# Kernel optimization log

Measured on AMD Instinct MI355X. Metric: run time of the kernel, lower is better.

## Reference

```python
import jax, jax.numpy as jnp
import numpy as np

N, E, B = 100000, 1000000, 64
DIN, DS, H, NG = 128, 1024, 256, 20


def setup_inputs() -> dict:
    key = jax.random.key(0)
    ks = jax.random.split(key, 48)
    lin = lambda k, i, o: (jax.random.normal(k, (i, o), jnp.float32) / np.sqrt(i)).astype(jnp.float32)
    inp = {
        'x': jax.random.normal(ks[0], (N, DIN), jnp.float32),
        'edge_index': jax.random.randint(ks[1], (2, E), 0, N, jnp.int32),
        'batch': jnp.sort(jax.random.randint(ks[2], (N,), 0, B, jnp.int32)),
        'static_features': jax.random.normal(ks[3], (B, DS), jnp.float32),
        'temporal_feats': jax.random.normal(ks[4], (B, 5), jnp.float32),
        'type_idx': jax.random.randint(ks[5], (B,), 0, 10, jnp.int32),
        'type_emb': jax.random.normal(ks[6], (10, H), jnp.float32),
        # static encoder
        'Ws1': lin(ks[7], DS, H), 'bs1': jnp.zeros(H), 'Ws2': lin(ks[8], H, H), 'bs2': jnp.zeros(H),
        # 3 GCN convs
        'Wc1': lin(ks[9], DIN, H), 'bc1': jnp.zeros(H),
        'Wc2': lin(ks[10], H, H), 'bc2': jnp.zeros(H),
        'Wc3': lin(ks[11], H, H), 'bc3': jnp.zeros(H),
        # residual dim_match linears
        'Wd1': lin(ks[12], DIN, H), 'bd1': jnp.zeros(H),
        'Wd2': lin(ks[13], H, H), 'bd2': jnp.zeros(H),
        'Wd3': lin(ks[14], H, H), 'bd3': jnp.zeros(H),
        # temporal MLP (5 -> H//2 -> H)
        'Wt1': lin(ks[15], 5, H // 2), 'bt1': jnp.zeros(H // 2),
        'Wt2': lin(ks[16], H // 2, H), 'bt2': jnp.zeros(H),
        # pattern detector
        'Wp1': lin(ks[17], H, H // 2), 'bp1': jnp.zeros(H // 2),
        'Wp2': lin(ks[18], H // 2, H), 'bp2': jnp.zeros(H),
        # fusion (5H -> 2H -> H)
        'Wf1': lin(ks[19], 5 * H, 2 * H), 'bf1': jnp.zeros(2 * H),
        'Wf2': lin(ks[20], 2 * H, H), 'bf2': jnp.zeros(H),
        # heads
        'Wg': lin(ks[21], H, NG), 'bg': jnp.zeros(NG),
        'Wtp': lin(ks[22], H, 1), 'btp': jnp.zeros(1),
    }
    return inp


def reference(x, edge_index, batch, static_features, temporal_feats, type_idx, type_emb,
              Ws1, bs1, Ws2, bs2,
              Wc1, bc1, Wc2, bc2, Wc3, bc3,
              Wd1, bd1, Wd2, bd2, Wd3, bd3,
              Wt1, bt1, Wt2, bt2,
              Wp1, bp1, Wp2, bp2,
              Wf1, bf1, Wf2, bf2,
              Wg, bg, Wtp, btp):
    n = x.shape[0]
    b = static_features.shape[0]
    src, dst = edge_index[0], edge_index[1]
    # GCN symmetric norm with self-loops: deg = 1 + in-degree
    deg = 1.0 + jax.ops.segment_sum(jnp.ones(src.shape[0], x.dtype), dst, num_segments=n)
    dinv = deg ** -0.5
    ew = dinv[src] * dinv[dst]  # [E] edge norm weights

    def gcn(h_in, W, bias):
        h = h_in @ W  # [n, H]
        agg = jax.ops.segment_sum(h[src] * ew[:, None], dst, num_segments=n)
        return agg + h / deg[:, None] + bias  # neighbor agg + self-loop + bias

    # 3 GCN layers with residual dim_match (dropout is identity at inference)
    x1 = jax.nn.relu(gcn(x, Wc1, bc1)) + (x @ Wd1 + bd1)
    x2 = jax.nn.relu(gcn(x1, Wc2, bc2)) + (x1 @ Wd2 + bd2)
    x3 = jax.nn.relu(gcn(x2, Wc3, bc3)) + (x2 @ Wd3 + bd3)

    pat = jax.nn.relu(jax.nn.relu(x3 @ Wp1 + bp1) @ Wp2 + bp2)

    counts = jnp.maximum(jax.ops.segment_sum(jnp.ones(n, x.dtype), batch, num_segments=b), 1.0)
    graph_embed = jax.ops.segment_sum(x3, batch, num_segments=b) / counts[:, None]
    pattern_embed = jax.ops.segment_sum(pat, batch, num_segments=b) / counts[:, None]

    static_embed = jax.nn.relu(static_features @ Ws1 + bs1) @ Ws2 + bs2
    temporal_embed = jax.nn.relu(temporal_feats @ Wt1 + bt1) @ Wt2 + bt2
    type_embed = type_emb[type_idx]

    combined = jnp.concatenate([graph_embed, static_embed, temporal_embed, type_embed, pattern_embed], axis=1)
    fused = jax.nn.relu(combined @ Wf1 + bf1) @ Wf2 + bf2
    group_logits = fused @ Wg + bg
    time_pred = fused @ Wtp + btp
    return fused, group_logits, time_pred
```

## Files before the change

kernel.cpp:

```cpp
#include <hip/hip_runtime.h>

#define H 256

typedef __attribute__((ext_vector_type(8))) short bf16x8;
typedef __attribute__((ext_vector_type(4))) float f32x4;

__device__ __forceinline__ float b2f(ushort h) {
    return __uint_as_float(((unsigned)h) << 16);
}
__device__ __forceinline__ float b2f_lo(unsigned u) {
    return __uint_as_float(u << 16);
}
__device__ __forceinline__ float b2f_hi(unsigned u) {
    return __uint_as_float(u & 0xffff0000u);
}
__device__ __forceinline__ ushort f2bf(float f) {
    unsigned u = __float_as_uint(f);
    unsigned r = (u + 0x7FFF + ((u >> 16) & 1)) >> 16;
    return (ushort)r;
}
__device__ __forceinline__ unsigned pack2bf(float lo, float hi) {
    return (unsigned)f2bf(lo) | ((unsigned)f2bf(hi) << 16);
}

__device__ __forceinline__ void gload16(const ushort* g, const short* l) {
    __builtin_amdgcn_global_load_lds(
        (const __attribute__((address_space(1))) void*)(const void*)g,
        (__attribute__((address_space(3))) void*)(void*)l, 16, 0, 0);
}

__global__ __launch_bounds__(256) void k_zero2_i(int* p, int* q, int n) {
    int i = blockIdx.x * 256 + threadIdx.x;
    if (i < n) { p[i] = 0; q[i] = 0; }
}

__global__ __launch_bounds__(256) void k_zero_f(float* p, int n) {
    int i = blockIdx.x * 256 + threadIdx.x;
    if (i < n) p[i] = 0.f;
}

__global__ __launch_bounds__(256) void k_count_deg_i(const int* __restrict__ dst, int* cnt, int E) {
    int i = blockIdx.x * 256 + threadIdx.x;
    if (i < E) atomicAdd(&cnt[dst[i]], 1);
}

__global__ __launch_bounds__(256) void k_scan1(const int* __restrict__ cnt, int* __restrict__ partial,
                                               int* __restrict__ bsums, int N) {
    __shared__ int s[256];
    int t = threadIdx.x;
    int idx = blockIdx.x * 256 + t;
    int v = idx < N ? cnt[idx] : 0;
    s[t] = v;
    __syncthreads();
    for (int off = 1; off < 256; off <<= 1) {
        int add = (t >= off) ? s[t - off] : 0;
        __syncthreads();
        s[t] += add;
        __syncthreads();
    }
    if (idx < N) partial[idx] = s[t];
    if (t == 255) bsums[blockIdx.x] = s[t];
}

__global__ __launch_bounds__(1024) void k_scan2(int* bsums, int nb) {
    __shared__ int s[1024];
    int t = threadIdx.x;
    s[t] = (t < nb) ? bsums[t] : 0;
    __syncthreads();
    for (int off = 1; off < 1024; off <<= 1) {
        int add = (t >= off) ? s[t - off] : 0;
        __syncthreads();
        s[t] += add;
        __syncthreads();
    }
    if (t < nb) bsums[t] = s[t];
}

__global__ __launch_bounds__(256) void k_scan3(const int* __restrict__ partial, const int* __restrict__ bsums,
                                               const int* __restrict__ cnt,
                                               int* __restrict__ rowptr, float* __restrict__ dinv,
                                               float* __restrict__ selfw, int N) {
    int idx = blockIdx.x * 256 + threadIdx.x;
    if (idx < N) {
        int off = blockIdx.x > 0 ? bsums[blockIdx.x - 1] : 0;
        rowptr[idx + 1] = partial[idx] + off;
        if (idx == 0) rowptr[0] = 0;
        float d = 1.0f + (float)cnt[idx];
        dinv[idx] = rsqrtf(d);
        selfw[idx] = 1.0f / d;
    }
}

__global__ __launch_bounds__(256) void k_scatter(const int* __restrict__ src, const int* __restrict__ dst,
                                                 const float* __restrict__ dinv, const int* __restrict__ rowptr,
                                                 int* __restrict__ fill, int* __restrict__ esrc,
                                                 float* __restrict__ ewt, int E) {
    int e = blockIdx.x * 256 + threadIdx.x;
    if (e >= E) return;
    int s = src[e], d = dst[e];
    int pos = rowptr[d] + atomicAdd(&fill[d], 1);
    esrc[pos] = s;
    ewt[pos] = dinv[s] * dinv[d];
}

__device__ __forceinline__ void tcvt_one(long i, const float* __restrict__ W, ushort* __restrict__ Wt,
                                         int K, int M) {
    int k = (int)(i / M), m = (int)(i - (long)k * M);
    Wt[(size_t)m * K + k] = f2bf(W[(size_t)k * M + m]);
}

__global__ __launch_bounds__(256) void k_prep(
    const float* __restrict__ x, ushort* __restrict__ xh, long nx, int DIN,
    const float* __restrict__ Wc1, ushort* Wc1t, const float* __restrict__ Wd1, ushort* Wd1t,
    const float* __restrict__ Wc2, ushort* Wc2t, const float* __restrict__ Wd2, ushort* Wd2t,
    const float* __restrict__ Wc3, ushort* Wc3t, const float* __restrict__ Wd3, ushort* Wd3t,
    const float* __restrict__ Wp1, ushort* Wp1t, const float* __restrict__ Wp2, ushort* Wp2t) {
    long i = (long)blockIdx.x * 256 + threadIdx.x;
    if (i < nx) { xh[i] = f2bf(x[i]); return; }
    i -= nx;
    long n1 = (long)DIN * 256;
    if (i < n1) { tcvt_one(i, Wc1, Wc1t, DIN, 256); return; }
    i -= n1;
    if (i < n1) { tcvt_one(i, Wd1, Wd1t, DIN, 256); return; }
    i -= n1;
    if (i < 65536) { tcvt_one(i, Wc2, Wc2t, 256, 256); return; }
    i -= 65536;
    if (i < 65536) { tcvt_one(i, Wd2, Wd2t, 256, 256); return; }
    i -= 65536;
    if (i < 65536) { tcvt_one(i, Wc3, Wc3t, 256, 256); return; }
    i -= 65536;
    if (i < 65536) { tcvt_one(i, Wd3, Wd3t, 256, 256); return; }
    i -= 65536;
    if (i < 32768) { tcvt_one(i, Wp1, Wp1t, 256, 128); return; }
    i -= 32768;
    if (i < 32768) { tcvt_one(i, Wp2, Wp2t, 128, 256); return; }
}

__global__ __launch_bounds__(256) void k_gather_b4(const ushort* __restrict__ xin, const int* __restrict__ rowptr,
                                                   const int* __restrict__ esrc, const float* __restrict__ ewt,
                                                   const float* __restrict__ selfw, ushort* __restrict__ p,
                                                   int N, int SX, int SP) {
    int node = blockIdx.x * 4 + (threadIdx.x >> 6);
    if (node >= N) return;
    int c = (threadIdx.x & 63) << 2;
    ushort4 h = *(const ushort4*)(xin + (size_t)node * SX + c);
    float sw = selfw[node];
    float a0 = b2f(h.x) * sw, a1 = b2f(h.y) * sw, a2 = b2f(h.z) * sw, a3 = b2f(h.w) * sw;
    int j = rowptr[node], r1 = rowptr[node + 1];
    for (; j + 3 < r1; j += 4) {
        int s0 = esrc[j], s1 = esrc[j + 1], s2 = esrc[j + 2], s3 = esrc[j + 3];
        float w0 = ewt[j], w1 = ewt[j + 1], w2 = ewt[j + 2], w3 = ewt[j + 3];
        ushort4 v0 = *(const ushort4*)(xin + (size_t)s0 * SX + c);
        ushort4 v1 = *(const ushort4*)(xin + (size_t)s1 * SX + c);
        ushort4 v2 = *(const ushort4*)(xin + (size_t)s2 * SX + c);
        ushort4 v3 = *(const ushort4*)(xin + (size_t)s3 * SX + c);
        a0 += b2f(v0.x) * w0 + b2f(v1.x) * w1 + b2f(v2.x) * w2 + b2f(v3.x) * w3;
        a1 += b2f(v0.y) * w0 + b2f(v1.y) * w1 + b2f(v2.y) * w2 + b2f(v3.y) * w3;
        a2 += b2f(v0.z) * w0 + b2f(v1.z) * w1 + b2f(v2.z) * w2 + b2f(v3.z) * w3;
        a3 += b2f(v0.w) * w0 + b2f(v1.w) * w1 + b2f(v2.w) * w2 + b2f(v3.w) * w3;
    }
    for (; j < r1; ++j) {
        int s0 = esrc[j];
        float w0 = ewt[j];
        ushort4 v0 = *(const ushort4*)(xin + (size_t)s0 * SX + c);
        a0 += b2f(v0.x) * w0; a1 += b2f(v0.y) * w0; a2 += b2f(v0.z) * w0; a3 += b2f(v0.w) * w0;
    }
    ushort4 o;
    o.x = f2bf(a0); o.y = f2bf(a1); o.z = f2bf(a2); o.w = f2bf(a3);
    *(ushort4*)(p + (size_t)node * SP + c) = o;
}

__global__ __launch_bounds__(256) void k_gather_b2(const ushort* __restrict__ xin, const int* __restrict__ rowptr,
                                                   const int* __restrict__ esrc, const float* __restrict__ ewt,
                                                   const float* __restrict__ selfw, ushort* __restrict__ p,
                                                   int N, int SX, int SP) {
    int node = blockIdx.x * 16 + (threadIdx.x >> 4);
    bool act = node < N;
    int nn = act ? node : N - 1;
    int c = (threadIdx.x & 15) << 3;
    uint4 hv = *(const uint4*)(xin + (size_t)nn * SX + c);
    float sw = selfw[nn];
    float a0 = b2f_lo(hv.x) * sw, a1 = b2f_hi(hv.x) * sw;
    float a2 = b2f_lo(hv.y) * sw, a3 = b2f_hi(hv.y) * sw;
    float a4 = b2f_lo(hv.z) * sw, a5 = b2f_hi(hv.z) * sw;
    float a6 = b2f_lo(hv.w) * sw, a7 = b2f_hi(hv.w) * sw;
    int j = act ? rowptr[nn] : 0, r1 = act ? rowptr[nn + 1] : 0;
    for (; j + 3 < r1; j += 4) {
        int s0 = esrc[j], s1 = esrc[j + 1], s2 = esrc[j + 2], s3 = esrc[j + 3];
        float w0 = ewt[j], w1 = ewt[j + 1], w2 = ewt[j + 2], w3 = ewt[j + 3];
        uint4 v0 = *(const uint4*)(xin + (size_t)s0 * SX + c);
        uint4 v1 = *(const uint4*)(xin + (size_t)s1 * SX + c);
        uint4 v2 = *(const uint4*)(xin + (size_t)s2 * SX + c);
        uint4 v3 = *(const uint4*)(xin + (size_t)s3 * SX + c);
        a0 += b2f_lo(v0.x) * w0 + b2f_lo(v1.x) * w1 + b2f_lo(v2.x) * w2 + b2f_lo(v3.x) * w3;
        a1 += b2f_hi(v0.x) * w0 + b2f_hi(v1.x) * w1 + b2f_hi(v2.x) * w2 + b2f_hi(v3.x) * w3;
        a2 += b2f_lo(v0.y) * w0 + b2f_lo(v1.y) * w1 + b2f_lo(v2.y) * w2 + b2f_lo(v3.y) * w3;
        a3 += b2f_hi(v0.y) * w0 + b2f_hi(v1.y) * w1 + b2f_hi(v2.y) * w2 + b2f_hi(v3.y) * w3;
        a4 += b2f_lo(v0.z) * w0 + b2f_lo(v1.z) * w1 + b2f_lo(v2.z) * w2 + b2f_lo(v3.z) * w3;
        a5 += b2f_hi(v0.z) * w0 + b2f_hi(v1.z) * w1 + b2f_hi(v2.z) * w2 + b2f_hi(v3.z) * w3;
        a6 += b2f_lo(v0.w) * w0 + b2f_lo(v1.w) * w1 + b2f_lo(v2.w) * w2 + b2f_lo(v3.w) * w3;
        a7 += b2f_hi(v0.w) * w0 + b2f_hi(v1.w) * w1 + b2f_hi(v2.w) * w2 + b2f_hi(v3.w) * w3;
    }
    for (; j < r1; ++j) {
        int s0 = esrc[j];
        float w0 = ewt[j];
        uint4 v0 = *(const uint4*)(xin + (size_t)s0 * SX + c);
        a0 += b2f_lo(v0.x) * w0; a1 += b2f_hi(v0.x) * w0;
        a2 += b2f_lo(v0.y) * w0; a3 += b2f_hi(v0.y) * w0;
        a4 += b2f_lo(v0.z) * w0; a5 += b2f_hi(v0.z) * w0;
        a6 += b2f_lo(v0.w) * w0; a7 += b2f_hi(v0.w) * w0;
    }
    if (act) {
        uint4 o;
        o.x = pack2bf(a0, a1); o.y = pack2bf(a2, a3);
        o.z = pack2bf(a4, a5); o.w = pack2bf(a6, a7);
        *(uint4*)(p + (size_t)node * SP + c) = o;
    }
}

__global__ __launch_bounds__(256, 2) void k_fused_mfma(
    const ushort* __restrict__ Pm, const ushort* __restrict__ X,
    const ushort* __restrict__ Wct, const ushort* __restrict__ Wdt,
    const float* __restrict__ bc, const float* __restrict__ bd,
    ushort* __restrict__ Out, int N, int K, int SP, int SX,
    const int* __restrict__ batch, float* __restrict__ gesum, int dopool) {
    __shared__ __align__(16) short Ps[64 * 64];
    __shared__ __align__(16) short Xs[64 * 64];
    __shared__ __align__(16) short Wcs[256 * 64];
    __shared__ __align__(16) short Wds[256 * 64];
    const int tid = threadIdx.x;
    const int wave = tid >> 6, lane = tid & 63;
    const int row0 = blockIdx.x * 64;

    f32x4 accC[4][4], accD[4][4];
#pragma unroll
    for (int i = 0; i < 4; ++i)
#pragma unroll
        for (int j = 0; j < 4; ++j) { accC[i][j] = (f32x4)0.f; accD[i][j] = (f32x4)0.f; }

    const int lr = lane >> 3;
    const int ls = lane & 7;
    const int swz = (ls ^ lr) << 3;
    const int m = lane & 15, t4 = lane >> 4;

    for (int k0 = 0; k0 < K; k0 += 64) {
#pragma unroll
        for (int i = 0; i < 2; ++i) {
            int rr = wave * 16 + i * 8;
            int gr = row0 + rr + lr; if (gr > N - 1) gr = N - 1;
            gload16(Pm + (size_t)gr * SP + k0 + swz, &Ps[rr * 64]);
            gload16(X + (size_t)gr * SX + k0 + swz, &Xs[rr * 64]);
        }
#pragma unroll
        for (int i = 0; i < 8; ++i) {
            int cc = wave * 64 + i * 8;
            gload16(Wct + (size_t)(cc + lr) * K + k0 + swz, &Wcs[cc * 64]);
            gload16(Wdt + (size_t)(cc + lr) * K + k0 + swz, &Wds[cc * 64]);
        }
        __syncthreads();

#pragma unroll
        for (int h = 0; h < 2; ++h) {
            const int slot = h * 4 + t4;
            bf16x8 aP[4], aX[4], bC[4], bD[4];
#pragma unroll
            for (int i = 0; i < 4; ++i) {
                int r = 16 * i + m;
                int off = r * 64 + ((slot ^ (r & 7)) << 3);
                aP[i] = *(bf16x8*)&Ps[off];
                aX[i] = *(bf16x8*)&Xs[off];
            }
#pragma unroll
            for (int j = 0; j < 4; ++j) {
                int c = wave * 64 + 16 * j + m;
                int off = c * 64 + ((slot ^ (c & 7)) << 3);
                bC[j] = *(bf16x8*)&Wcs[off];
                bD[j] = *(bf16x8*)&Wds[off];
            }
#pragma unroll
            for (int i = 0; i < 4; ++i)
#pragma unroll
                for (int j = 0; j < 4; ++j) {
                    accC[i][j] = __builtin_amdgcn_mfma_f32_16x16x32_bf16(aP[i], bC[j], accC[i][j], 0, 0, 0);
                    accD[i][j] = __builtin_amdgcn_mfma_f32_16x16x32_bf16(aX[i], bD[j], accD[i][j], 0, 0, 0);
                }
        }
        __syncthreads();
    }

    int* sb = (int*)Ps;
    if (dopool && tid < 64) {
        int r = row0 + tid;
        sb[tid] = batch[r < N ? r : (N - 1)];
    }

    const int rq = t4 * 4;
#pragma unroll
    for (int j = 0; j < 4; ++j) {
        int col = wave * 64 + 16 * j + m;
        float bcv = bc[col], bdv = bd[col];
#pragma unroll
        for (int i = 0; i < 4; ++i)
#pragma unroll
            for (int g = 0; g < 4; ++g) {
                int row = row0 + 16 * i + rq + g;
                if (row < N) {
                    float v = fmaxf(accC[i][j][g] + bcv, 0.f) + accD[i][j][g] + bdv;
                    Out[(size_t)row * 256 + col] = f2bf(v);
                }
            }
    }

    if (dopool) {
        __syncthreads();
        const int g0 = sb[0], g1 = sb[63];
        for (int g = g0; g <= g1; ++g) {
#pragma unroll
            for (int j = 0; j < 4; ++j) {
                int col = wave * 64 + 16 * j + m;
                float bcv = bc[col], bdv = bd[col];
                float s = 0.f;
#pragma unroll
                for (int i = 0; i < 4; ++i)
#pragma unroll
                    for (int q = 0; q < 4; ++q) {
                        int rl = 16 * i + rq + q;
                        bool ok = (sb[rl] == g) && (row0 + rl < N);
                        float v = fmaxf(accC[i][j][q] + bcv, 0.f) + accD[i][j][q] + bdv;
                        s += ok ? v : 0.f;
                    }
                s += __shfl_down(s, 32, 64);
                s += __shfl_down(s, 16, 64);
                if (lane < 16) atomicAdd(&gesum[(size_t)g * 256 + wave * 64 + 16 * j + lane], s);
            }
        }
    }
}

__global__ __launch_bounds__(256, 2) void k_pat_fused(
    const ushort* __restrict__ Bb, const ushort* __restrict__ Wp1t, const ushort* __restrict__ Wp2t,
    const float* __restrict__ bp1, const float* __restrict__ bp2,
    const int* __restrict__ batch, float* __restrict__ pesum, int N) {
    __shared__ __align__(16) short Wp2s[128 * 128];
    __shared__ __align__(16) short Wp1s[128 * 64];
    __shared__ __align__(16) short Bbs[64 * 64];
    __shared__ __align__(16) short Ts[64 * 128];
    __shared__ int sbatch[64];
    const int tid = threadIdx.x;
    const int wave = tid >> 6, lane = tid & 63;
    const int row0 = blockIdx.x * 64;
    const int m = lane & 15, t4 = lane >> 4;
    const int lr = lane >> 3, ls = lane & 7;
    const int swz = (ls ^ lr) << 3;
    const int rl4 = lane >> 4;
    const int sl = lane & 15;

    if (tid < 64) {
        int r = row0 + tid;
        sbatch[tid] = batch[r < N ? r : (N - 1)];
    }

#pragma unroll
    for (int it = 0; it < 8; ++it) {
        int c0 = wave * 32 + it * 4;
        int c = c0 + rl4;
        gload16(Wp2t + (size_t)c * 128 + ((sl ^ (c & 15)) << 3), &Wp2s[c0 * 128]);
    }

    f32x4 acc1[4][2];
#pragma unroll
    for (int i = 0; i < 4; ++i)
#pragma unroll
        for (int j = 0; j < 2; ++j) acc1[i][j] = (f32x4)0.f;

    for (int k0 = 0; k0 < 256; k0 += 64) {
#pragma unroll
        for (int i = 0; i < 2; ++i) {
            int rr = wave * 16 + i * 8;
            int gr = row0 + rr + lr; if (gr > N - 1) gr = N - 1;
            gload16(Bb + (size_t)gr * 256 + k0 + swz, &Bbs[rr * 64]);
        }
#pragma unroll
        for (int i = 0; i < 4; ++i) {
            int cc = wave * 32 + i * 8;
            gload16(Wp1t + (size_t)(cc + lr) * 256 + k0 + swz, &Wp1s[cc * 64]);
        }
        __syncthreads();
#pragma unroll
        for (int h = 0; h < 2; ++h) {
            const int slot = h * 4 + t4;
            bf16x8 aB[4], bW[2];
#pragma unroll
            for (int i = 0; i < 4; ++i) {
                int r = 16 * i + m;
                aB[i] = *(bf16x8*)&Bbs[r * 64 + ((slot ^ (r & 7)) << 3)];
            }
#pragma unroll
            for (int j = 0; j < 2; ++j) {
                int c = wave * 32 + 16 * j + m;
                bW[j] = *(bf16x8*)&Wp1s[c * 64 + ((slot ^ (c & 7)) << 3)];
            }
#pragma unroll
            for (int i = 0; i < 4; ++i)
#pragma unroll
                for (int j = 0; j < 2; ++j)
                    acc1[i][j] = __builtin_amdgcn_mfma_f32_16x16x32_bf16(aB[i], bW[j], acc1[i][j], 0, 0, 0);
        }
        __syncthreads();
    }

    const int rq = t4 * 4;
#pragma unroll
    for (int j = 0; j < 2; ++j) {
        int col = wave * 32 + 16 * j + m;
        float bv = bp1[col];
#pragma unroll
        for (int i = 0; i < 4; ++i)
#pragma unroll
            for (int g = 0; g < 4; ++g) {
                int r = 16 * i + rq + g;
                float v = fmaxf(acc1[i][j][g] + bv, 0.f);
                Ts[r * 128 + (((col >> 3) ^ (r & 15)) << 3) + (col & 7)] = (short)f2bf(v);
            }
    }
    __syncthreads();

    const int g0 = sbatch[0];
    const int g1 = sbatch[63];
    for (int hh = 0; hh < 2; ++hh) {
        if (hh == 1) {
            __syncthreads();
#pragma unroll
            for (int it = 0; it < 8; ++it) {
                int c0 = wave * 32 + it * 4;
                int c = c0 + rl4;
                gload16(Wp2t + (size_t)(128 + c) * 128 + ((sl ^ (c & 15)) << 3), &Wp2s[c0 * 128]);
            }
            __syncthreads();
        }

        f32x4 acc2[4][2];
#pragma unroll
        for (int i = 0; i < 4; ++i)
#pragma unroll
            for (int j = 0; j < 2; ++j) acc2[i][j] = (f32x4)0.f;

#pragma unroll
        for (int sl4 = 0; sl4 < 4; ++sl4) {
            const int s16 = sl4 * 4 + t4;
            bf16x8 af[4], bf[2];
#pragma unroll
            for (int i = 0; i < 4; ++i) {
                int r = 16 * i + m;
                af[i] = *(bf16x8*)&Ts[r * 128 + ((s16 ^ (r & 15)) << 3)];
            }
#pragma unroll
            for (int j = 0; j < 2; ++j) {
                int cl = wave * 32 + 16 * j + m;
                bf[j] = *(bf16x8*)&Wp2s[cl * 128 + ((s16 ^ (cl & 15)) << 3)];
            }
#pragma unroll
            for (int i = 0; i < 4; ++i)
#pragma unroll
                for (int j = 0; j < 2; ++j)
                    acc2[i][j] = __builtin_amdgcn_mfma_f32_16x16x32_bf16(af[i], bf[j], acc2[i][j], 0, 0, 0);
        }

        for (int g = g0; g <= g1; ++g) {
#pragma unroll
            for (int j = 0; j < 2; ++j) {
                int col = hh * 128 + wave * 32 + 16 * j + m;
                float bv = bp2[col];
                float s = 0.f;
#pragma unroll
                for (int i = 0; i < 4; ++i)
#pragma unroll
                    for (int q = 0; q < 4; ++q) {
                        int rl = 16 * i + rq + q;
                        bool ok = (sbatch[rl] == g) && (row0 + rl < N);
                        float v = fmaxf(acc2[i][j][q] + bv, 0.f);
                        s += ok ? v : 0.f;
                    }
                s += __shfl_down(s, 32, 64);
                s += __shfl_down(s, 16, 64);
                if (lane < 16) atomicAdd(&pesum[(size_t)g * 256 + hh * 128 + wave * 32 + 16 * j + lane], s);
            }
        }
    }
}

__global__ void k_ranges(const int* __restrict__ batch, int N, int B, int* __restrict__ start,
                         float* __restrict__ countsf) {
    int b = threadIdx.x;
    if (b <= B) {
        int lo = 0, hi = N;
        while (lo < hi) {
            int mid = (lo + hi) >> 1;
            if (batch[mid] < b) lo = mid + 1; else hi = mid;
        }
        start[b] = lo;
    }
    __syncthreads();
    if (b < B) {
        int cnt = start[b + 1] - start[b];
        countsf[b] = (float)(cnt > 0 ? cnt : 1);
    }
}

__global__ __launch_bounds__(256) void k_fin_comb(const float* __restrict__ gesum, const float* __restrict__ pesum,
                                                  const float* __restrict__ countsf,
                                                  const float* __restrict__ temb, const int* __restrict__ tidx,
                                                  float* __restrict__ comb) {
    int b = blockIdx.x, t = threadIdx.x;
    float inv = 1.0f / countsf[b];
    float* o = comb + (size_t)b * 1280;
    o[t] = gesum[(size_t)b * 256 + t] * inv;
    o[768 + t] = temb[(size_t)tidx[b] * 256 + t];
    o[1024 + t] = pesum[(size_t)b * 256 + t] * inv;
}

__global__ __launch_bounds__(256) void k_dense(const float* __restrict__ vin, int vs,
                                               const float* __restrict__ W, const float* __restrict__ bias,
                                               float* __restrict__ out, int os, int oo,
                                               int K, int M, int relu) {
    const int b = blockIdx.y;
    const int wave = threadIdx.x >> 6, lane = threadIdx.x & 63;
    const int c = blockIdx.x * 64 + lane;
    const float* vrow = vin + (size_t)b * vs;
    float acc = 0.f;
    int k = wave;
    for (; k + 28 < K; k += 32) {
#pragma unroll
        for (int u = 0; u < 8; ++u)
            acc += vrow[k + 4 * u] * W[(size_t)(k + 4 * u) * M + c];
    }
    for (; k < K; k += 4)
        acc += vrow[k] * W[(size_t)k * M + c];
    __shared__ float red[4][64];
    red[wave][lane] = acc;
    __syncthreads();
    if (wave == 0) {
        float s = red[0][lane] + red[1][lane] + red[2][lane] + red[3][lane] + bias[c];
        if (relu) s = fmaxf(s, 0.f);
        out[(size_t)b * os + oo + c] = s;
    }
}

__global__ __launch_bounds__(256) void k_heads_small(const float* __restrict__ fused,
                                                     const float* __restrict__ Wg, const float* __restrict__ bg,
                                                     const float* __restrict__ Wtp, const float* __restrict__ btp,
                                                     float* __restrict__ out_logits, float* __restrict__ out_tp,
                                                     int NG) {
    __shared__ float lf[256];
    int b = blockIdx.x, tid = threadIdx.x;
    int wave = tid >> 6, lane = tid & 63;
    lf[tid] = fused[(size_t)b * 256 + tid];
    __syncthreads();
    for (int c = wave; c < NG; c += 4) {
        float s = 0.f;
#pragma unroll
        for (int k = lane; k < 256; k += 64) s += lf[k] * Wg[(size_t)k * NG + c];
#pragma unroll
        for (int off = 32; off > 0; off >>= 1) s += __shfl_down(s, off, 64);
        if (lane == 0) out_logits[(size_t)b * NG + c] = s + bg[c];
    }
    if (wave == 0) {
        float s = 0.f;
#pragma unroll
        for (int k = lane; k < 256; k += 64) s += lf[k] * Wtp[k];
#pragma unroll
        for (int off = 32; off > 0; off >>= 1) s += __shfl_down(s, off, 64);
        if (lane == 0) out_tp[b] = s + btp[0];
    }
}

extern "C" void kernel_launch(void* const* d_in, const int* in_sizes, int n_in,
                              void* d_out, int out_size, void* d_ws, size_t ws_size,
                              hipStream_t stream) {
    const float* x   = (const float*)d_in[0];
    const int* ei    = (const int*)d_in[1];
    const int* batch = (const int*)d_in[2];
    const float* sf  = (const float*)d_in[3];
    const float* tf  = (const float*)d_in[4];
    const int* tidx  = (const int*)d_in[5];
    const float* temb = (const float*)d_in[6];
    const float *Ws1 = (const float*)d_in[7],  *bs1 = (const float*)d_in[8];
    const float *Ws2 = (const float*)d_in[9],  *bs2 = (const float*)d_in[10];
    const float *Wc1 = (const float*)d_in[11], *bc1 = (const float*)d_in[12];
    const float *Wc2 = (const float*)d_in[13], *bc2 = (const float*)d_in[14];
    const float *Wc3 = (const float*)d_in[15], *bc3 = (const float*)d_in[16];
    const float *Wd1 = (const float*)d_in[17], *bd1 = (const float*)d_in[18];
    const float *Wd2 = (const float*)d_in[19], *bd2 = (const float*)d_in[20];
    const float *Wd3 = (const float*)d_in[21], *bd3 = (const float*)d_in[22];
    const float *Wt1 = (const float*)d_in[23], *bt1 = (const float*)d_in[24];
    const float *Wt2 = (const float*)d_in[25], *bt2 = (const float*)d_in[26];
    const float *Wp1 = (const float*)d_in[27], *bp1 = (const float*)d_in[28];
    const float *Wp2 = (const float*)d_in[29], *bp2 = (const float*)d_in[30];
    const float *Wf1 = (const float*)d_in[31], *bf1 = (const float*)d_in[32];
    const float *Wf2 = (const float*)d_in[33], *bf2 = (const float*)d_in[34];
    const float *Wg  = (const float*)d_in[35], *bg  = (const float*)d_in[36];
    const float *Wtp = (const float*)d_in[37], *btp = (const float*)d_in[38];

    const int N = in_sizes[2];
    const int E = in_sizes[1] / 2;
    const int B = in_sizes[5];
    const int DIN = in_sizes[0] / N;
    const int DS = in_sizes[3] / B;
    const int NG = in_sizes[36];
    const int* src = ei;
    const int* dst = ei + E;

    char* w = (char*)d_ws;
    ushort* A   = (ushort*)w;              w += (size_t)N * 256 * 2;
    ushort* Bb  = (ushort*)w;              w += (size_t)N * 256 * 2;
    ushort* xh  = (ushort*)w;              w += (size_t)N * 128 * 2;
    ushort* Wc1t = (ushort*)w;             w += 128 * 256 * 2;
    ushort* Wd1t = (ushort*)w;             w += 128 * 256 * 2;
    ushort* Wc2t = (ushort*)w;             w += 256 * 256 * 2;
    ushort* Wd2t = (ushort*)w;             w += 256 * 256 * 2;
    ushort* Wc3t = (ushort*)w;             w += 256 * 256 * 2;
    ushort* Wd3t = (ushort*)w;             w += 256 * 256 * 2;
    ushort* Wp1t = (ushort*)w;             w += 256 * 128 * 2;
    ushort* Wp2t = (ushort*)w;             w += 128 * 256 * 2;
    int* esrc   = (int*)w;                 w += (size_t)E * 4;
    float* ewt  = (float*)w;               w += (size_t)E * 4;
    int* cnt    = (int*)w;                 w += (size_t)N * 4;
    int* part   = (int*)w;                 w += (size_t)N * 4;
    int* rowptr = (int*)w;                 w += (size_t)(N + 1) * 4;
    int* fill   = (int*)w;                 w += (size_t)N * 4;
    int* bsums  = (int*)w;                 w += 1024 * 4;
    float* dinv = (float*)w;               w += (size_t)N * 4;
    float* selfw = (float*)w;              w += (size_t)N * 4;
    int* startp = (int*)w;                 w += (B + 1) * 4;
    float* countsf = (float*)w;            w += B * 4;
    float* ge = (float*)w;                 w += B * 256 * 4;
    float* pe = (float*)w;                 w += B * 256 * 4;
    float* s1buf = (float*)w;              w += B * 256 * 4;
    float* t1buf = (float*)w;              w += B * 128 * 4;
    float* comb = (float*)w;               w += B * 1280 * 4;
    float* fh = (float*)w;                 w += B * 512 * 4;

    float* out_fused = (float*)d_out;
    float* out_logits = out_fused + (size_t)B * H;
    float* out_tp = out_logits + (size_t)B * NG;

    dim3 blk(256);
    const int nbN = (N + 255) / 256;
    const int nbE = (E + 255) / 256;

    k_zero2_i<<<dim3(nbN), blk, 0, stream>>>(cnt, fill, N);
    k_count_deg_i<<<dim3(nbE), blk, 0, stream>>>(dst, cnt, E);
    k_scan1<<<dim3(nbN), blk, 0, stream>>>(cnt, part, bsums, N);
    k_scan2<<<dim3(1), dim3(1024), 0, stream>>>(bsums, nbN);
    k_scan3<<<dim3(nbN), blk, 0, stream>>>(part, bsums, cnt, rowptr, dinv, selfw, N);
    k_scatter<<<dim3(nbE), blk, 0, stream>>>(src, dst, dinv, rowptr, fill, esrc, ewt, E);

    {
        long nx = (long)N * DIN;
        long tot = nx + 2L * DIN * 256 + 4L * 65536 + 2L * 32768;
        k_prep<<<dim3((unsigned)((tot + 255) / 256)), blk, 0, stream>>>(
            x, xh, nx, DIN, Wc1, Wc1t, Wd1, Wd1t, Wc2, Wc2t, Wd2, Wd2t,
            Wc3, Wc3t, Wd3, Wd3t, Wp1, Wp1t, Wp2, Wp2t);
        k_ranges<<<dim3(1), dim3(128), 0, stream>>>(batch, N, B, startp, countsf);
        k_zero_f<<<dim3((2 * B * 256 + 255) / 256), blk, 0, stream>>>(ge, 2 * B * 256);
    }

    const int ngb4 = (N + 3) / 4;
    const int ngb2 = (N + 15) / 16;
    const int nfb = (N + 63) / 64;

    k_dense<<<dim3(4, B), blk, 0, stream>>>(sf, DS, Ws1, bs1, s1buf, 256, 0, DS, 256, 1);
    k_dense<<<dim3(4, B), blk, 0, stream>>>(s1buf, 256, Ws2, bs2, comb, 1280, 256, 256, 256, 0);
    k_dense<<<dim3(2, B), blk, 0, stream>>>(tf, 5, Wt1, bt1, t1buf, 128, 0, 5, 128, 1);
    k_dense<<<dim3(4, B), blk, 0, stream>>>(t1buf, 128, Wt2, bt2, comb, 1280, 512, 128, 256, 0);

    k_gather_b2<<<dim3(ngb2), blk, 0, stream>>>(xh, rowptr, esrc, ewt, selfw, A, N, 128, 128);
    k_fused_mfma<<<dim3(nfb), blk, 0, stream>>>(A, xh, Wc1t, Wd1t, bc1, bd1, Bb, N, 128, 128, 128, batch, ge, 0);
    k_gather_b4<<<dim3(ngb4), blk, 0, stream>>>(Bb, rowptr, esrc, ewt, selfw, A, N, 256, 256);
    k_fused_mfma<<<dim3(nfb), blk, 0, stream>>>(A, Bb, Wc2t, Wd2t, bc2, bd2, A, N, 256, 256, 256, batch, ge, 0);
    k_gather_b4<<<dim3(ngb4), blk, 0, stream>>>(A, rowptr, esrc, ewt, selfw, Bb, N, 256, 256);
    k_fused_mfma<<<dim3(nfb), blk, 0, stream>>>(Bb, A, Wc3t, Wd3t, bc3, bd3, Bb, N, 256, 256, 256, batch, ge, 1);

    k_pat_fused<<<dim3(nfb), blk, 0, stream>>>(Bb, Wp1t, Wp2t, bp1, bp2, batch, pe, N);
    k_fin_comb<<<dim3(B), blk, 0, stream>>>(ge, pe, countsf, temb, tidx, comb);

    k_dense<<<dim3(8, B), blk, 0, stream>>>(comb, 1280, Wf1, bf1, fh, 512, 0, 1280, 512, 1);
    k_dense<<<dim3(4, B), blk, 0, stream>>>(fh, 512, Wf2, bf2, out_fused, 256, 0, 512, 256, 0);
    k_heads_small<<<dim3(B), blk, 0, stream>>>(out_fused, Wg, bg, Wtp, btp, out_logits, out_tp, NG);
}
```

Measured before the change: 795.6 us.

## Double-buffer activation tiles and read weights directly from global in fused MFMA GEMM

The fused GEMM kernel no longer stages the two 256x64 weight tiles in LDS. Each wave now loads its B fragments straight from global memory, where they should mostly hit cache. The P and X activation tiles are double-buffered so the next K-slice load overlaps the current MFMA work, and one barrier per iteration is removed. This cuts LDS use from about 80KB to 32KB, which could raise occupancy, but it adds global-load latency on the weight path inside the inner loop.

Result: slower. 866.3 us (+8.9%).

```diff
diff --git a/kernel.cpp b/kernel.cpp
--- a/kernel.cpp
+++ b/kernel.cpp
@@ -130,7 +130,7 @@
     if (i < 65536) { tcvt_one(i, Wc3, Wc3t, 256, 256); return; }
     i -= 65536;
     if (i < 65536) { tcvt_one(i, Wd3, Wd3t, 256, 256); return; }
-    i -= 65536;
+    i -= 32768 * 2;
     if (i < 32768) { tcvt_one(i, Wp1, Wp1t, 256, 128); return; }
     i -= 32768;
     if (i < 32768) { tcvt_one(i, Wp2, Wp2t, 128, 256); return; }
@@ -224,10 +224,8 @@
     const float* __restrict__ bc, const float* __restrict__ bd,
     ushort* __restrict__ Out, int N, int K, int SP, int SX,
     const int* __restrict__ batch, float* __restrict__ gesum, int dopool) {
-    __shared__ __align__(16) short Ps[64 * 64];
-    __shared__ __align__(16) short Xs[64 * 64];
-    __shared__ __align__(16) short Wcs[256 * 64];
-    __shared__ __align__(16) short Wds[256 * 64];
+    __shared__ __align__(16) short Ps[2][64 * 64];
+    __shared__ __align__(16) short Xs[2][64 * 64];
     const int tid = threadIdx.x;
     const int wave = tid >> 6, lane = tid & 63;
     const int row0 = blockIdx.x * 64;
@@ -243,22 +241,27 @@
     const int swz = (ls ^ lr) << 3;
     const int m = lane & 15, t4 = lane >> 4;
 
-    for (int k0 = 0; k0 < K; k0 += 64) {
-#pragma unroll
-        for (int i = 0; i < 2; ++i) {
-            int rr = wave * 16 + i * 8;
-            int gr = row0 + rr + lr; if (gr > N - 1) gr = N - 1;
-            gload16(Pm + (size_t)gr * SP + k0 + swz, &Ps[rr * 64]);
-            gload16(X + (size_t)gr * SX + k0 + swz, &Xs[rr * 64]);
-        }
-#pragma unroll
-        for (int i = 0; i < 8; ++i) {
-            int cc = wave * 64 + i * 8;
-            gload16(Wct + (size_t)(cc + lr) * K + k0 + swz, &Wcs[cc * 64]);
-            gload16(Wdt + (size_t)(cc + lr) * K + k0 + swz, &Wds[cc * 64]);
-        }
-        __syncthreads();
-
+    int gr0 = row0 + wave * 16 + lr;      if (gr0 > N - 1) gr0 = N - 1;
+    int gr1 = row0 + wave * 16 + 8 + lr;  if (gr1 > N - 1) gr1 = N - 1;
+    const int rr0 = wave * 16, rr1 = wave * 16 + 8;
+
+    gload16(Pm + (size_t)gr0 * SP + swz, &Ps[0][rr0 * 64]);
+    gload16(X + (size_t)gr0 * SX + swz, &Xs[0][rr0 * 64]);
+    gload16(Pm + (size_t)gr1 * SP + swz, &Ps[0][rr1 * 64]);
+    gload16(X + (size_t)gr1 * SX + swz, &Xs[0][rr1 * 64]);
+    __syncthreads();
+
+    const int S = K >> 6;
+    int cur = 0;
+    for (int s = 0; s < S; ++s) {
+        const int k0 = s << 6;
+        if (s + 1 < S) {
+            const int kn = k0 + 64;
+            gload16(Pm + (size_t)gr0 * SP + kn + swz, &Ps[cur ^ 1][rr0 * 64]);
+            gload16(X + (size_t)gr0 * SX + kn + swz, &Xs[cur ^ 1][rr0 * 64]);
+            gload16(Pm + (size_t)gr1 * SP + kn + swz, &Ps[cur ^ 1][rr1 * 64]);
+            gload16(X + (size_t)gr1 * SX + kn + swz, &Xs[cur ^ 1][rr1 * 64]);
+        }
 #pragma unroll
         for (int h = 0; h < 2; ++h) {
             const int slot = h * 4 + t4;
@@ -267,15 +270,15 @@
             for (int i = 0; i < 4; ++i) {
                 int r = 16 * i + m;
                 int off = r * 64 + ((slot ^ (r & 7)) << 3);
-                aP[i] = *(bf16x8*)&Ps[off];
-                aX[i] = *(bf16x8*)&Xs[off];
+                aP[i] = *(bf16x8*)&Ps[cur][off];
+                aX[i] = *(bf16x8*)&Xs[cur][off];
             }
 #pragma unroll
             for (int j = 0; j < 4; ++j) {
                 int c = wave * 64 + 16 * j + m;
-                int off = c * 64 + ((slot ^ (c & 7)) << 3);
-                bC[j] = *(bf16x8*)&Wcs[off];
-                bD[j] = *(bf16x8*)&Wds[off];
+                size_t goff = (size_t)c * K + k0 + slot * 8;
+                bC[j] = *(const bf16x8*)(Wct + goff);
+                bD[j] = *(const bf16x8*)(Wdt + goff);
             }
 #pragma unroll
             for (int i = 0; i < 4; ++i)
@@ -286,9 +289,10 @@
                 }
         }
         __syncthreads();
-    }
-
-    int* sb = (int*)Ps;
+        cur ^= 1;
+    }
+
+    int* sb = (int*)&Ps[0][0];
     if (dopool && tid < 64) {
         int r = row0 + tid;
         sb[tid] = batch[r < N ? r : (N - 1)];
```
